# Kernel optimization log

Hardware: AMD Instinct MI355X
Metric: run time of the kernel (lower is better)

The kernel has to match this reference:

```python
import jax, jax.numpy as jnp
import numpy as np

D, L, C, CP, H, HD, QB, KB = 8, 2048, 128, 16, 4, 32, 32, 128
NQ = L // QB

def _ln(x, eps=1e-5):
    m = jnp.mean(x, axis=-1, keepdims=True)
    v = jnp.var(x, axis=-1, keepdims=True)
    return (x - m) * jax.lax.rsqrt(v + eps)

def _ada_ln(a, s, Wg, bg, Ws):
    # AF3 AdaLN: gated layernorm conditioned on s
    an = _ln(a); sn = _ln(s)
    return jax.nn.sigmoid(sn @ Wg + bg) * an + sn @ Ws

def setup_inputs() -> dict:
    key = jax.random.key(0)
    ks = jax.random.split(key, 32)
    p = lambda i, shape: jax.random.normal(ks[i], shape, dtype=jnp.float32) * 0.02
    inp = {}
    inp['A_I'] = jax.random.normal(ks[0], (D, L, C), dtype=jnp.float32)
    inp['S_I'] = jax.random.normal(ks[1], (D, L, C), dtype=jnp.float32)
    inp['Z_II'] = jax.random.normal(ks[2], (1, L, L, CP), dtype=jnp.float32)
    # static sliding-window indices: 128-key window centered on each 32-query block
    inp['indicesQ'] = jnp.arange(L, dtype=jnp.int64).reshape(NQ, QB)
    kraw = (jnp.arange(NQ) * QB - (KB - QB) // 2)[:, None] + jnp.arange(KB)[None, :]
    inp['indicesK'] = jnp.clip(kraw, 0, L - 1).astype(jnp.int64)
    inp['maskQ_float'] = jnp.zeros((NQ, QB), jnp.float32)
    inp['maskK_float'] = ((kraw < 0) | (kraw >= L)).astype(jnp.float32)
    # parameters
    inp['ada1_Wg'] = p(3, (C, C)); inp['ada1_bg'] = jnp.zeros((C,), jnp.float32); inp['ada1_Ws'] = p(4, (C, C))
    inp['Wq'] = p(5, (C, H * HD)); inp['bq'] = jnp.zeros((H * HD,), jnp.float32)
    inp['Wk'] = p(6, (C, H * HD)); inp['Wv'] = p(7, (C, H * HD))
    inp['ln0_g'] = jnp.ones((CP,), jnp.float32); inp['ln0_b'] = jnp.zeros((CP,), jnp.float32)
    inp['Wb'] = p(8, (CP, H))
    inp['Wg_attn'] = p(9, (C, H * HD))
    inp['Wa'] = p(10, (H * HD, C))
    inp['Wop'] = p(11, (C, C)); inp['bop'] = jnp.full((C,), -2.0, jnp.float32)
    inp['ada2_Wg'] = p(12, (C, C)); inp['ada2_bg'] = jnp.zeros((C,), jnp.float32); inp['ada2_Ws'] = p(13, (C, C))
    inp['W_sw'] = p(14, (C, 2 * C)); inp['W_lin'] = p(15, (C, 2 * C))
    inp['ct_Wg'] = p(16, (C, C)); inp['ct_bg'] = jnp.full((C,), -2.0, jnp.float32)
    inp['W_out2'] = p(17, (2 * C, C))
    return inp

def _forward(A_I, S_I, Z_II, indicesQ, indicesK, maskQ_float, maskK_float,
             ada1_Wg, ada1_bg, ada1_Ws, Wq, bq, Wk, Wv, ln0_g, ln0_b, Wb,
             Wg_attn, Wa, Wop, bop, ada2_Wg, ada2_bg, ada2_Ws, W_sw, W_lin,
             ct_Wg, ct_bg, W_out2):
    Dn, Lv = A_I.shape[0], A_I.shape[1]
    An = _ada_ln(A_I, S_I, ada1_Wg, ada1_bg, ada1_Ws)
    Q = (An @ Wq + bq).reshape(Dn, Lv, H, HD)
    K = (An @ Wk).reshape(Dn, Lv, H, HD)
    V = (An @ Wv).reshape(Dn, Lv, H, HD)
    B = ((_ln(Z_II) * ln0_g + ln0_b) @ Wb)[0]        # [L, L, H]
    G = jax.nn.sigmoid(An @ Wg_attn).reshape(Dn, Lv, H, HD)
    qs = Q[:, indicesQ]                              # [D, nq, qb, H, hd]
    ksub = K[:, indicesK]                            # [D, nq, kb, H, hd]
    vs = V[:, indicesK]
    attn = jnp.einsum('dnihc,dnjhc->dnijh', qs, ksub) / jnp.sqrt(jnp.float32(HD))
    bias = B[indicesQ[:, :, None], indicesK[:, None, :]]  # [nq, qb, kb, H]
    attn = attn + bias[None]
    mask = maskQ_float[None, :, :, None, None] + maskK_float[None, :, None, :, None]
    attn = attn - 1e9 * mask
    attn = jax.nn.softmax(attn, axis=-2)             # softmax over key window (j)
    af = jnp.einsum('dnijh,dnjhc->dnihc', attn, vs)
    af = af * (1.0 - maskQ_float)[None, :, :, None, None]
    af = af.reshape(Dn, -1, H, HD)[:, :Lv]
    af = (G * af).reshape(Dn, Lv, H * HD) @ Wa
    B_I = jax.nn.sigmoid(S_I @ Wop + bop) * af
    A = A_I + B_I
    an2 = _ada_ln(A, S_I, ada2_Wg, ada2_bg, ada2_Ws)
    b = jax.nn.silu(an2 @ W_sw) * (an2 @ W_lin)      # SwiGLU transition
    A = A + jax.nn.sigmoid(S_I @ ct_Wg + ct_bg) * (b @ W_out2)
    return A

def reference(A_I, S_I, Z_II, indicesQ, indicesK, maskQ_float, maskK_float,
              ada1_Wg, ada1_bg, ada1_Ws, Wq, bq, Wk, Wv, ln0_g, ln0_b, Wb,
              Wg_attn, Wa, Wop, bop, ada2_Wg, ada2_bg, ada2_Ws, W_sw, W_lin,
              ct_Wg, ct_bg, W_out2):
    return _forward(A_I, S_I, Z_II, indicesQ, indicesK, maskQ_float, maskK_float,
                    ada1_Wg, ada1_bg, ada1_Ws, Wq, bq, Wk, Wv, ln0_g, ln0_b, Wb,
                    Wg_attn, Wa, Wop, bop, ada2_Wg, ada2_bg, ada2_Ws, W_sw, W_lin,
                    ct_Wg, ct_bg, W_out2)
```

## Files before the change

### kernel.cpp

```cpp
#include <hip/hip_runtime.h>

#define DL 16384
#define LL 2048
#define NQB 64
#define QBS 32
#define KBS 128

typedef __attribute__((ext_vector_type(8))) short short8;
typedef __attribute__((ext_vector_type(4))) short short4v;
typedef __attribute__((ext_vector_type(4))) float f32x4;

__device__ __forceinline__ float sigmoidf_(float x) { return 1.f / (1.f + expf(-x)); }

__device__ __forceinline__ short f2bf(float f) {
    union { float f; unsigned u; } v; v.f = f;
    unsigned r = (v.u + 0x7FFFu + ((v.u >> 16) & 1u)) >> 16;
    return (short)r;
}
__device__ __forceinline__ float bf2f(short h) {
    union { unsigned u; float f; } v; v.u = ((unsigned)(unsigned short)h) << 16;
    return v.f;
}
__device__ __forceinline__ unsigned packbf16(short a, short b) {
    return ((unsigned)(unsigned short)a) | (((unsigned)(unsigned short)b) << 16);
}

#define AFRAG(buf, stride, r0, kk) (*(const short8*)&(buf)[(size_t)((r0) + cl) * (stride) + (kk) * 32 + kg * 8])
#define WFRAG(Wt, K, n0, kk) (*(const short8*)((Wt) + (size_t)((n0) + cl) * (K) + (kk) * 32 + kg * 8))
#define MFMA(acc, a, b) acc = __builtin_amdgcn_mfma_f32_16x16x32_bf16(a, b, acc, 0, 0, 0)

__global__ __launch_bounds__(256) void k_prep(
    const float* __restrict__ W0, const float* __restrict__ W1, const float* __restrict__ W2,
    const float* __restrict__ W3, const float* __restrict__ W4, const float* __restrict__ W5,
    const float* __restrict__ W6, const float* __restrict__ W7, const float* __restrict__ W8,
    const float* __restrict__ W9, const float* __restrict__ W10,
    const float* __restrict__ Wsw, const float* __restrict__ Wlin, const float* __restrict__ Wout2,
    const float* __restrict__ Z, const float* __restrict__ g16, const float* __restrict__ b16,
    const float* __restrict__ Wb,
    short* __restrict__ wout, short* __restrict__ BBt)
{
    __shared__ float sW[128 * 128];
    __shared__ float sWb[64], sg[16], sb[16];
    __shared__ short sT[4 * 4 * 128];
    const int b = blockIdx.x;
    const int tid = threadIdx.x;

    if (b < 17) {
        const float* srcs[14] = {W0,W1,W2,W3,W4,W5,W6,W7,W8,W9,W10,Wsw,Wlin,Wout2};
        const int sel[17]  = {0,1,2,3,4,5,6,7,8,9,10,11,11,12,12,13,13};
        const int soff[17] = {0,0,0,0,0,0,0,0,0,0,0, 0,128, 0,128, 0,16384};
        const int sN[17]   = {128,128,128,128,128,128,128,128,128,128,128, 256,256,256,256, 128,128};
        const int doff[17] = {0,16384,32768,49152,65536,81920,98304,114688,131072,147456,163840,
                              180224,196608, 212992,229376, 245760,245888};
        const int dK[17]   = {128,128,128,128,128,128,128,128,128,128,128, 128,128,128,128, 256,256};
        const float* src = srcs[sel[b]] + soff[b];
        const int srcN = sN[b];
        short* dst = wout + doff[b];
        const int dstK = dK[b];
        {
            const int r = tid >> 1, ch = (tid & 1) * 64;
            #pragma unroll
            for (int u = 0; u < 16; ++u) {
                float4 v = *(const float4*)(src + (size_t)r * srcN + ch + u * 4);
                *(float4*)&sW[r * 128 + ch + u * 4] = v;
            }
        }
        __syncthreads();
        {
            const int o = tid >> 1, kh = (tid & 1) * 64;
            #pragma unroll
            for (int u8 = 0; u8 < 8; ++u8) {
                short8 pk;
                #pragma unroll
                for (int e = 0; e < 8; ++e)
                    pk[e] = f2bf(sW[(kh + u8 * 8 + e) * 128 + o]);
                *(short8*)(dst + (size_t)o * dstK + kh + u8 * 8) = pk;
            }
        }
    } else {
        const int bb = b - 17;
        const int n = bb >> 3;
        const int io = (bb & 7) * 4;
        if (tid < 64) sWb[tid] = Wb[tid];
        if (tid < 16) { sg[tid] = g16[tid]; sb[tid] = b16[tid]; }
        __syncthreads();
        #pragma unroll
        for (int p = 0; p < 2; ++p) {
            int pair = tid + 256 * p;
            int il = pair >> 7, j = pair & 127;
            int i = io + il;
            int kr = n * 32 - 48 + j;
            int kc = min(max(kr, 0), LL - 1);
            const float4* z4 = (const float4*)(Z + ((long)(n * 32 + i) * LL + kc) * 16);
            float zv[16];
            #pragma unroll
            for (int w = 0; w < 4; ++w) {
                float4 v = z4[w];
                zv[w * 4 + 0] = v.x; zv[w * 4 + 1] = v.y; zv[w * 4 + 2] = v.z; zv[w * 4 + 3] = v.w;
            }
            float sm = 0.f, sq = 0.f;
            #pragma unroll
            for (int cp = 0; cp < 16; ++cp) { sm += zv[cp]; sq = fmaf(zv[cp], zv[cp], sq); }
            float m = sm * (1.f / 16.f);
            float rs = rsqrtf(sq * (1.f / 16.f) - m * m + 1e-5f);
            float b0 = 0.f, b1 = 0.f, b2 = 0.f, b3 = 0.f;
            #pragma unroll
            for (int cp = 0; cp < 16; ++cp) {
                float zn = (zv[cp] - m) * rs * sg[cp] + sb[cp];
                b0 = fmaf(zn, sWb[cp * 4 + 0], b0);
                b1 = fmaf(zn, sWb[cp * 4 + 1], b1);
                b2 = fmaf(zn, sWb[cp * 4 + 2], b2);
                b3 = fmaf(zn, sWb[cp * 4 + 3], b3);
            }
            sT[(0 * 4 + il) * 128 + j] = f2bf(b0);
            sT[(1 * 4 + il) * 128 + j] = f2bf(b1);
            sT[(2 * 4 + il) * 128 + j] = f2bf(b2);
            sT[(3 * 4 + il) * 128 + j] = f2bf(b3);
        }
        __syncthreads();
        #pragma unroll
        for (int rr = 0; rr < 2; ++rr) {
            int cid = tid + rr * 256;
            int hh = cid >> 7, rem = cid & 127;
            int il = rem >> 5, jb = (rem & 31) * 4;
            short4v pk = *(const short4v*)&sT[(hh * 4 + il) * 128 + jb];
            *(short4v*)(BBt + (((size_t)n * 4 + hh) * 32 + io + il) * 128 + jb) = pk;
        }
    }
}

__global__ __launch_bounds__(512) void k_adaln_qkvg(
    const float* __restrict__ A_I, const float* __restrict__ S_I,
    const short* __restrict__ Wg1t, const short* __restrict__ Ws1t,
    const short* __restrict__ Wqt, const short* __restrict__ Wkt,
    const short* __restrict__ Wvt, const short* __restrict__ Wgat,
    const float* __restrict__ bg1, const float* __restrict__ bq,
    short* __restrict__ Qo, short* __restrict__ Ko, short* __restrict__ Vo, short* __restrict__ Go)
{
    __shared__ short sAr[32 * 136];
    __shared__ short sSn[32 * 136];
    __shared__ short sAn[32 * 136];
    __shared__ float sMean[32], sRstd[32];
    const int tid = threadIdx.x;
    const int lane = tid & 63;
    const long t0 = (long)blockIdx.x * 32;

    {
        const int row = tid >> 4, seg = tid & 15;
        const float* ap = A_I + (t0 + row) * 128 + seg * 8;
        const float* sp = S_I + (t0 + row) * 128 + seg * 8;
        float av[8], sv[8];
        #pragma unroll
        for (int u = 0; u < 2; ++u) {
            float4 a4 = ((const float4*)ap)[u];
            float4 s4 = ((const float4*)sp)[u];
            av[4*u] = a4.x; av[4*u+1] = a4.y; av[4*u+2] = a4.z; av[4*u+3] = a4.w;
            sv[4*u] = s4.x; sv[4*u+1] = s4.y; sv[4*u+2] = s4.z; sv[4*u+3] = s4.w;
        }
        float am = 0.f, aq = 0.f, sm = 0.f, sq = 0.f;
        #pragma unroll
        for (int u = 0; u < 8; ++u) {
            am += av[u]; aq = fmaf(av[u], av[u], aq);
            sm += sv[u]; sq = fmaf(sv[u], sv[u], sq);
        }
        am += __shfl_xor(am, 1); am += __shfl_xor(am, 2); am += __shfl_xor(am, 4); am += __shfl_xor(am, 8);
        aq += __shfl_xor(aq, 1); aq += __shfl_xor(aq, 2); aq += __shfl_xor(aq, 4); aq += __shfl_xor(aq, 8);
        sm += __shfl_xor(sm, 1); sm += __shfl_xor(sm, 2); sm += __shfl_xor(sm, 4); sm += __shfl_xor(sm, 8);
        sq += __shfl_xor(sq, 1); sq += __shfl_xor(sq, 2); sq += __shfl_xor(sq, 4); sq += __shfl_xor(sq, 8);
        float amean = am * (1.f / 128.f);
        float arstd = rsqrtf(aq * (1.f / 128.f) - amean * amean + 1e-5f);
        float smean = sm * (1.f / 128.f);
        float srstd = rsqrtf(sq * (1.f / 128.f) - smean * smean + 1e-5f);
        if ((tid & 15) == 0) { sMean[row] = amean; sRstd[row] = arstd; }
        short8 pa, ps;
        #pragma unroll
        for (int e = 0; e < 8; ++e) {
            pa[e] = f2bf(av[e]);
            ps[e] = f2bf((sv[e] - smean) * srstd);
        }
        *(short8*)&sAr[row * 136 + seg * 8] = pa;
        *(short8*)&sSn[row * 136 + seg * 8] = ps;
    }
    __syncthreads();
    const int w = tid >> 6;
    const int n0 = w * 16;
    const int cl = lane & 15, kg = lane >> 4;
    {
        short8 wg[4], wsf[4];
        #pragma unroll
        for (int kk = 0; kk < 4; ++kk) {
            wg[kk]  = WFRAG(Wg1t, 128, n0, kk);
            wsf[kk] = WFRAG(Ws1t, 128, n0, kk);
        }
        #pragma unroll
        for (int mt = 0; mt < 2; ++mt) {
            f32x4 ag = {0.f, 0.f, 0.f, 0.f}, as = {0.f, 0.f, 0.f, 0.f};
            #pragma unroll
            for (int kk = 0; kk < 4; ++kk) {
                short8 a = AFRAG(sSn, 136, mt * 16, kk);
                MFMA(ag, wg[kk], a);
                MFMA(as, wsf[kk], a);
            }
            const int tok = mt * 16 + cl;
            const int c0 = n0 + kg * 4;
            float4 bg4 = *(const float4*)&bg1[c0];
            float mean = sMean[tok], rstd = sRstd[tok];
            short4v ar4 = *(const short4v*)&sAr[tok * 136 + c0];
            short4v o;
            #pragma unroll
            for (int i = 0; i < 4; ++i) {
                float an = (bf2f(ar4[i]) - mean) * rstd;
                float An = sigmoidf_(ag[i] + ((const float*)&bg4)[i]) * an + as[i];
                o[i] = f2bf(An);
            }
            *(short4v*)&sAn[tok * 136 + c0] = o;
        }
    }
    __syncthreads();
    {
        const float SCL = 0.17677669529663687f;
        short8 af[2][4];
        #pragma unroll
        for (int mt = 0; mt < 2; ++mt)
            #pragma unroll
            for (int kk = 0; kk < 4; ++kk)
                af[mt][kk] = AFRAG(sAn, 136, mt * 16, kk);
        const int c0 = n0 + kg * 4;
        float4 bq4 = *(const float4*)&bq[c0];
        #pragma unroll
        for (int m = 0; m < 4; ++m) {
            const short* Wt = (m == 0) ? Wqt : (m == 1) ? Wkt : (m == 2) ? Wvt : Wgat;
            short8 wf[4];
            #pragma unroll
            for (int kk = 0; kk < 4; ++kk) wf[kk] = WFRAG(Wt, 128, n0, kk);
            #pragma unroll
            for (int mt = 0; mt < 2; ++mt) {
                f32x4 acc = {0.f, 0.f, 0.f, 0.f};
                #pragma unroll
                for (int kk = 0; kk < 4; ++kk) MFMA(acc, wf[kk], af[mt][kk]);
                long t = t0 + mt * 16 + cl;
                short4v o;
                if (m == 0) {
                    #pragma unroll
                    for (int i = 0; i < 4; ++i) o[i] = f2bf((acc[i] + ((const float*)&bq4)[i]) * SCL);
                    *(short4v*)(Qo + t * 128 + c0) = o;
                } else if (m == 1) {
                    #pragma unroll
                    for (int i = 0; i < 4; ++i) o[i] = f2bf(acc[i]);
                    *(short4v*)(Ko + t * 128 + c0) = o;
                } else if (m == 2) {
                    #pragma unroll
                    for (int i = 0; i < 4; ++i) o[i] = f2bf(acc[i]);
                    *(short4v*)(Vo + t * 128 + c0) = o;
                } else {
                    #pragma unroll
                    for (int i = 0; i < 4; ++i) o[i] = f2bf(sigmoidf_(acc[i]));
                    *(short4v*)(Go + t * 128 + c0) = o;
                }
            }
        }
    }
}

__global__ __launch_bounds__(512) void k_attn_postf(
    const short* __restrict__ Qg, const short* __restrict__ Kg, const short* __restrict__ Vg,
    const short* __restrict__ Gg, const short* __restrict__ BBt, const float* __restrict__ maskK,
    const float* __restrict__ S_I, const float* __restrict__ A_I,
    const short* __restrict__ Wat, const short* __restrict__ Wopt, const short* __restrict__ ctWgt,
    const short* __restrict__ Wg2t, const short* __restrict__ Ws2t,
    const short* __restrict__ Wswt, const short* __restrict__ Wlint, const short* __restrict__ Wout2t,
    const float* __restrict__ bop, const float* __restrict__ ctbg, const float* __restrict__ bg2,
    float* __restrict__ Out)
{
    __shared__ __align__(16) char smem[78336];
    short* sAF  = (short*)smem;
    short* vts  = (short*)(smem + 8704);
    short* Pl   = (short*)(smem + 43520);
    short* sS   = (short*)(smem + 8704);
    short* sSn  = (short*)(smem + 17408);
    float* sA   = (float*)(smem + 26112);
    float* sMean = (float*)(smem + 43008);
    float* sRstd = (float*)(smem + 43136);
    short* sAn2 = sAF;
    short* sB   = (short*)(smem + 8704);

    const int n = blockIdx.x, d = blockIdx.y;
    const int tid = threadIdx.x;
    const int lane = tid & 63;
    const long tb = (long)d * LL;
    const long t0 = tb + n * 32;
    const int kbase = n * 32 - 48;
    const int cl = lane & 15, kg = lane >> 4;
    const int w = tid >> 6;
    const int h = w >> 1, amt = w & 1;

    {
        const int unit = tid >> 1, half = tid & 1;
        const int hh = unit >> 6, j0 = (unit & 63) * 2;
        int kc0 = min(max(kbase + j0, 0), LL - 1);
        int kc1 = min(max(kbase + j0 + 1, 0), LL - 1);
        const short8* p0 = (const short8*)(Vg + (tb + kc0) * 128 + hh * 32 + half * 16);
        const short8* p1 = (const short8*)(Vg + (tb + kc1) * 128 + hh * 32 + half * 16);
        short8 e0 = p0[0], e1 = p0[1];
        short8 o0 = p1[0], o1 = p1[1];
        short* vh = vts + hh * 4352;
        #pragma unroll
        for (int e = 0; e < 8; ++e)
            *(unsigned*)&vh[(half * 16 + e) * 136 + j0] = packbf16(e0[e], o0[e]);
        #pragma unroll
        for (int e = 0; e < 8; ++e)
            *(unsigned*)&vh[(half * 16 + 8 + e) * 136 + j0] = packbf16(e1[e], o1[e]);
    }

    float sc[8][4];
    {
        short8 qf = *(const short8*)(Qg + (t0 + amt * 16 + cl) * 128 + h * 32 + kg * 8);
        #pragma unroll
        for (int nt = 0; nt < 8; ++nt) {
            int kc = min(max(kbase + nt * 16 + cl, 0), LL - 1);
            short8 kf = *(const short8*)(Kg + (tb + kc) * 128 + h * 32 + kg * 8);
            f32x4 s = {0.f, 0.f, 0.f, 0.f};
            MFMA(s, kf, qf);
            float4 mk4 = *(const float4*)(maskK + n * 128 + nt * 16 + kg * 4);
            short4v bfr = *(const short4v*)(BBt + (((size_t)n * 4 + h) * 32 + amt * 16 + cl) * 128 + nt * 16 + kg * 4);
            #pragma unroll
            for (int i = 0; i < 4; ++i)
                sc[nt][i] = s[i] + bf2f(bfr[i]) - ((const float*)&mk4)[i] * 1e9f;
        }
    }
    {
        float mx = sc[0][0];
        #pragma unroll
        for (int nt = 0; nt < 8; ++nt)
            #pragma unroll
            for (int i = 0; i < 4; ++i) mx = fmaxf(mx, sc[nt][i]);
        mx = fmaxf(mx, __shfl_xor(mx, 16));
        mx = fmaxf(mx, __shfl_xor(mx, 32));
        float sm = 0.f;
        #pragma unroll
        for (int nt = 0; nt < 8; ++nt)
            #pragma unroll
            for (int i = 0; i < 4; ++i) {
                float p = __expf(sc[nt][i] - mx);
                sc[nt][i] = p; sm += p;
            }
        sm += __shfl_xor(sm, 16);
        sm += __shfl_xor(sm, 32);
        float inv = 1.f / sm;
        short* PH = Pl + h * 4352;
        const int tok = amt * 16 + cl;
        #pragma unroll
        for (int nt = 0; nt < 8; ++nt) {
            short4v p4;
            #pragma unroll
            for (int i = 0; i < 4; ++i) p4[i] = f2bf(sc[nt][i] * inv);
            *(short4v*)&PH[tok * 136 + nt * 16 + kg * 4] = p4;
        }
    }
    __syncthreads();
    {
        short* PH = Pl + h * 4352;
        short* vh = vts + h * 4352;
        const int tok = amt * 16 + cl;
        short8 pfr[4];
        #pragma unroll
        for (int kk = 0; kk < 4; ++kk)
            pfr[kk] = *(const short8*)&PH[tok * 136 + kk * 32 + kg * 8];
        #pragma unroll
        for (int ct = 0; ct < 2; ++ct) {
            f32x4 acc = {0.f, 0.f, 0.f, 0.f};
            #pragma unroll
            for (int kk = 0; kk < 4; ++kk) {
                short8 a = *(const short8*)&vh[(ct * 16 + cl) * 136 + kk * 32 + kg * 8];
                MFMA(acc, a, pfr[kk]);
            }
            const int c0 = h * 32 + ct * 16 + kg * 4;
            short4v g4 = *(const short4v*)(Gg + (t0 + tok) * 128 + c0);
            short4v o4;
            #pragma unroll
            for (int i = 0; i < 4; ++i) o4[i] = f2bf(bf2f(g4[i]) * acc[i]);
            *(short4v*)&sAF[tok * 136 + c0] = o4;
        }
    }
    __syncthreads();

    {
        const int row = tid >> 4, seg = tid & 15;
        const float* apI = A_I + (t0 + row) * 128 + seg * 8;
        #pragma unroll
        for (int u = 0; u < 2; ++u)
            *(float4*)&sA[row * 132 + seg * 8 + u * 4] = ((const float4*)apI)[u];
        const float* sp = S_I + (t0 + row) * 128 + seg * 8;
        float sv[8];
        #pragma unroll
        for (int u = 0; u < 2; ++u) {
            float4 s4 = ((const float4*)sp)[u];
            sv[4*u] = s4.x; sv[4*u+1] = s4.y; sv[4*u+2] = s4.z; sv[4*u+3] = s4.w;
        }
        float sm = 0.f, sq = 0.f;
        #pragma unroll
        for (int u = 0; u < 8; ++u) { sm += sv[u]; sq = fmaf(sv[u], sv[u], sq); }
        sm += __shfl_xor(sm, 1); sm += __shfl_xor(sm, 2); sm += __shfl_xor(sm, 4); sm += __shfl_xor(sm, 8);
        sq += __shfl_xor(sq, 1); sq += __shfl_xor(sq, 2); sq += __shfl_xor(sq, 4); sq += __shfl_xor(sq, 8);
        float smean = sm * (1.f / 128.f);
        float srstd = rsqrtf(sq * (1.f / 128.f) - smean * smean + 1e-5f);
        short8 pr, pn;
        #pragma unroll
        for (int e = 0; e < 8; ++e) {
            float s = sv[e];
            pr[e] = f2bf(s);
            pn[e] = f2bf((s - smean) * srstd);
        }
        *(short8*)&sS [row * 136 + seg * 8] = pr;
        *(short8*)&sSn[row * 136 + seg * 8] = pn;
    }
    __syncthreads();
    const int n0 = w * 16;
    const int c0 = n0 + kg * 4;
    float g2s[8];

    {
        short8 wA[4], wO[4], wG[4];
        #pragma unroll
        for (int kk = 0; kk < 4; ++kk) {
            wA[kk] = WFRAG(Wat, 128, n0, kk);
            wO[kk] = WFRAG(Wopt, 128, n0, kk);
            wG[kk] = WFRAG(ctWgt, 128, n0, kk);
        }
        float4 bop4 = *(const float4*)&bop[c0];
        float4 ct4  = *(const float4*)&ctbg[c0];
        #pragma unroll
        for (int rt = 0; rt < 2; ++rt) {
            f32x4 aA = {0.f,0.f,0.f,0.f}, aO = {0.f,0.f,0.f,0.f}, aG = {0.f,0.f,0.f,0.f};
            #pragma unroll
            for (int kk = 0; kk < 4; ++kk) {
                short8 af = AFRAG(sAF, 136, rt * 16, kk);
                short8 sf = AFRAG(sS, 136, rt * 16, kk);
                MFMA(aA, wA[kk], af);
                MFMA(aO, wO[kk], sf);
                MFMA(aG, wG[kk], sf);
            }
            const int tok = rt * 16 + cl;
            float4 Av = *(const float4*)&sA[tok * 132 + c0];
            float4 outv;
            #pragma unroll
            for (int i = 0; i < 4; ++i) {
                ((float*)&outv)[i] = ((const float*)&Av)[i]
                    + sigmoidf_(aO[i] + ((const float*)&bop4)[i]) * aA[i];
                g2s[rt * 4 + i] = sigmoidf_(aG[i] + ((const float*)&ct4)[i]);
            }
            *(float4*)&sA[tok * 132 + c0] = outv;
        }
    }
    __syncthreads();
    {
        const int row = tid >> 4, seg = tid & 15;
        float m = 0.f, q = 0.f;
        #pragma unroll
        for (int u = 0; u < 2; ++u) {
            float4 v = *(const float4*)&sA[row * 132 + seg * 8 + u * 4];
            m += v.x + v.y + v.z + v.w;
            q = fmaf(v.x, v.x, q); q = fmaf(v.y, v.y, q);
            q = fmaf(v.z, v.z, q); q = fmaf(v.w, v.w, q);
        }
        m += __shfl_xor(m, 1); m += __shfl_xor(m, 2); m += __shfl_xor(m, 4); m += __shfl_xor(m, 8);
        q += __shfl_xor(q, 1); q += __shfl_xor(q, 2); q += __shfl_xor(q, 4); q += __shfl_xor(q, 8);
        float mean = m * (1.f / 128.f);
        float rstd = rsqrtf(q * (1.f / 128.f) - mean * mean + 1e-5f);
        if ((tid & 15) == 0) { sMean[row] = mean; sRstd[row] = rstd; }
    }
    __syncthreads();
    {
        short8 wg2[4], ws2[4];
        #pragma unroll
        for (int kk = 0; kk < 4; ++kk) {
            wg2[kk] = WFRAG(Wg2t, 128, n0, kk);
            ws2[kk] = WFRAG(Ws2t, 128, n0, kk);
        }
        float4 bg24 = *(const float4*)&bg2[c0];
        #pragma unroll
        for (int rt = 0; rt < 2; ++rt) {
            f32x4 ag = {0.f,0.f,0.f,0.f}, as = {0.f,0.f,0.f,0.f};
            #pragma unroll
            for (int kk = 0; kk < 4; ++kk) {
                short8 a = AFRAG(sSn, 136, rt * 16, kk);
                MFMA(ag, wg2[kk], a);
                MFMA(as, ws2[kk], a);
            }
            const int tok = rt * 16 + cl;
            float mean = sMean[tok], rstd = sRstd[tok];
            float4 Av = *(const float4*)&sA[tok * 132 + c0];
            short4v o;
            #pragma unroll
            for (int i = 0; i < 4; ++i) {
                float lnA = (((const float*)&Av)[i] - mean) * rstd;
                o[i] = f2bf(sigmoidf_(ag[i] + ((const float*)&bg24)[i]) * lnA + as[i]);
            }
            *(short4v*)&sAn2[tok * 136 + c0] = o;
        }
    }
    __syncthreads();
    {
        short8 a2f[2][4];
        #pragma unroll
        for (int rt = 0; rt < 2; ++rt)
            #pragma unroll
            for (int kk = 0; kk < 4; ++kk)
                a2f[rt][kk] = AFRAG(sAn2, 136, rt * 16, kk);
        #pragma unroll
        for (int j = 0; j < 2; ++j) {
            const int n0b = w * 32 + j * 16;
            short8 ww[4], wl[4];
            #pragma unroll
            for (int kk = 0; kk < 4; ++kk) {
                ww[kk] = WFRAG(Wswt, 128, n0b, kk);
                wl[kk] = WFRAG(Wlint, 128, n0b, kk);
            }
            #pragma unroll
            for (int rt = 0; rt < 2; ++rt) {
                f32x4 aw = {0.f,0.f,0.f,0.f}, al = {0.f,0.f,0.f,0.f};
                #pragma unroll
                for (int kk = 0; kk < 4; ++kk) {
                    MFMA(aw, ww[kk], a2f[rt][kk]);
                    MFMA(al, wl[kk], a2f[rt][kk]);
                }
                const int tok = rt * 16 + cl;
                short4v o;
                #pragma unroll
                for (int i = 0; i < 4; ++i) {
                    float x = aw[i];
                    o[i] = f2bf((x / (1.f + expf(-x))) * al[i]);
                }
                *(short4v*)&sB[tok * 264 + n0b + kg * 4] = o;
            }
        }
    }
    __syncthreads();
    {
        short8 wo[8];
        #pragma unroll
        for (int kk = 0; kk < 8; ++kk) wo[kk] = WFRAG(Wout2t, 256, n0, kk);
        #pragma unroll
        for (int rt = 0; rt < 2; ++rt) {
            f32x4 acc = {0.f,0.f,0.f,0.f};
            #pragma unroll
            for (int kk = 0; kk < 8; ++kk) {
                short8 a = AFRAG(sB, 264, rt * 16, kk);
                MFMA(acc, wo[kk], a);
            }
            const int tok = rt * 16 + cl;
            float4 Av = *(const float4*)&sA[tok * 132 + c0];
            float4 outv;
            #pragma unroll
            for (int i = 0; i < 4; ++i)
                ((float*)&outv)[i] = ((const float*)&Av)[i] + g2s[rt * 4 + i] * acc[i];
            *(float4*)(Out + (t0 + tok) * 128 + c0) = outv;
        }
    }
}

extern "C" void kernel_launch(void* const* d_in, const int* in_sizes, int n_in,
                              void* d_out, int out_size, void* d_ws, size_t ws_size,
                              hipStream_t stream)
{
    const float* A_I  = (const float*)d_in[0];
    const float* S_I  = (const float*)d_in[1];
    const float* Z    = (const float*)d_in[2];
    const float* maskK = (const float*)d_in[6];
    const float* a1Wg = (const float*)d_in[7];
    const float* a1bg = (const float*)d_in[8];
    const float* a1Ws = (const float*)d_in[9];
    const float* Wq   = (const float*)d_in[10];
    const float* bq   = (const float*)d_in[11];
    const float* Wk   = (const float*)d_in[12];
    const float* Wv   = (const float*)d_in[13];
    const float* ln0g = (const float*)d_in[14];
    const float* ln0b = (const float*)d_in[15];
    const float* Wb   = (const float*)d_in[16];
    const float* Wga  = (const float*)d_in[17];
    const float* Wa   = (const float*)d_in[18];
    const float* Wop  = (const float*)d_in[19];
    const float* bop  = (const float*)d_in[20];
    const float* a2Wg = (const float*)d_in[21];
    const float* a2bg = (const float*)d_in[22];
    const float* a2Ws = (const float*)d_in[23];
    const float* Wsw  = (const float*)d_in[24];
    const float* Wlin = (const float*)d_in[25];
    const float* ctWg = (const float*)d_in[26];
    const float* ctbg = (const float*)d_in[27];
    const float* Wout2 = (const float*)d_in[28];
    float* out = (float*)d_out;

    const size_t NTC = (size_t)DL * 128;
    short* Qb = (short*)d_ws;
    short* Kb = Qb + NTC;
    short* Vb = Kb + NTC;
    short* Gb = Vb + NTC;
    short* BBt = Gb + NTC;
    short* wbt = BBt + (size_t)NQB * 4 * 32 * 128;

    short* Wg1t = wbt + 0 * 16384;
    short* Ws1t = wbt + 1 * 16384;
    short* Wqt  = wbt + 2 * 16384;
    short* Wkt  = wbt + 3 * 16384;
    short* Wvt  = wbt + 4 * 16384;
    short* Wgat = wbt + 5 * 16384;
    short* Wat  = wbt + 6 * 16384;
    short* Wopt = wbt + 7 * 16384;
    short* ctWgt = wbt + 8 * 16384;
    short* Wg2t = wbt + 9 * 16384;
    short* Ws2t = wbt + 10 * 16384;
    short* Wswt = wbt + 180224;
    short* Wlint = wbt + 212992;
    short* Wout2t = wbt + 245760;

    k_prep<<<529, 256, 0, stream>>>(a1Wg, a1Ws, Wq, Wk, Wv, Wga, Wa, Wop, ctWg,
                                    a2Wg, a2Ws, Wsw, Wlin, Wout2,
                                    Z, ln0g, ln0b, Wb, wbt, BBt);
    k_adaln_qkvg<<<DL / 32, 512, 0, stream>>>(A_I, S_I, Wg1t, Ws1t, Wqt, Wkt, Wvt, Wgat,
                                              a1bg, bq, Qb, Kb, Vb, Gb);
    k_attn_postf<<<dim3(NQB, 8), 512, 0, stream>>>(Qb, Kb, Vb, Gb, BBt, maskK,
                                                   S_I, A_I,
                                                   Wat, Wopt, ctWgt, Wg2t, Ws2t,
                                                   Wswt, Wlint, Wout2t,
                                                   bop, ctbg, a2bg, out);
}
```

Measured before the change: 71.22 us.

## Move pair-bias computation into the AdaLN/QKVG kernel and split off weight transpose

Splits the prep kernel in two. A small 17-block kernel now only transposes the weights. The Z pair-bias work (layernorm over 16 channels plus projection to 4 heads) moves into the AdaLN/QKV kernel as extra blocks 512..1023, using 512 threads per block with one pair per thread. The aim is to let the bias work overlap with the QKV projection and to shorten the serial prep kernel, though the extra blocks may compete for occupancy with the main work.

```diff
diff --git a/kernel.cpp b/kernel.cpp
--- a/kernel.cpp
+++ b/kernel.cpp
@@ -29,65 +29,80 @@
 #define WFRAG(Wt, K, n0, kk) (*(const short8*)((Wt) + (size_t)((n0) + cl) * (K) + (kk) * 32 + kg * 8))
 #define MFMA(acc, a, b) acc = __builtin_amdgcn_mfma_f32_16x16x32_bf16(a, b, acc, 0, 0, 0)
 
-__global__ __launch_bounds__(256) void k_prep(
+__global__ __launch_bounds__(256) void k_wtrans(
     const float* __restrict__ W0, const float* __restrict__ W1, const float* __restrict__ W2,
     const float* __restrict__ W3, const float* __restrict__ W4, const float* __restrict__ W5,
     const float* __restrict__ W6, const float* __restrict__ W7, const float* __restrict__ W8,
     const float* __restrict__ W9, const float* __restrict__ W10,
     const float* __restrict__ Wsw, const float* __restrict__ Wlin, const float* __restrict__ Wout2,
+    short* __restrict__ wout)
+{
+    __shared__ float sW[128 * 128];
+    const int b = blockIdx.x;
+    const int tid = threadIdx.x;
+    const float* srcs[14] = {W0,W1,W2,W3,W4,W5,W6,W7,W8,W9,W10,Wsw,Wlin,Wout2};
+    const int sel[17]  = {0,1,2,3,4,5,6,7,8,9,10,11,11,12,12,13,13};
+    const int soff[17] = {0,0,0,0,0,0,0,0,0,0,0, 0,128, 0,128, 0,16384};
+    const int sN[17]   = {128,128,128,128,128,128,128,128,128,128,128, 256,256,256,256, 128,128};
+    const int doff[17] = {0,16384,32768,49152,65536,81920,98304,114688,131072,147456,163840,
+                          180224,196608, 212992,229376, 245760,245888};
+    const int dK[17]   = {128,128,128,128,128,128,128,128,128,128,128, 128,128,128,128, 256,256};
+    const float* src = srcs[sel[b]] + soff[b];
+    const int srcN = sN[b];
+    short* dst = wout + doff[b];
+    const int dstK = dK[b];
+    {
+        const int r = tid >> 1, ch = (tid & 1) * 64;
+        #pragma unroll
+        for (int u = 0; u < 16; ++u) {
+            float4 v = *(const float4*)(src + (size_t)r * srcN + ch + u * 4);
+            *(float4*)&sW[r * 128 + ch + u * 4] = v;
+        }
+    }
+    __syncthreads();
+    {
+        const int o = tid >> 1, kh = (tid & 1) * 64;
+        #pragma unroll
+        for (int u8 = 0; u8 < 8; ++u8) {
+            short8 pk;
+            #pragma unroll
+            for (int e = 0; e < 8; ++e)
+                pk[e] = f2bf(sW[(kh + u8 * 8 + e) * 128 + o]);
+            *(short8*)(dst + (size_t)o * dstK + kh + u8 * 8) = pk;
+        }
+    }
+}
+
+__global__ __launch_bounds__(512) void k_main(
+    const float* __restrict__ A_I, const float* __restrict__ S_I,
+    const short* __restrict__ Wg1t, const short* __restrict__ Ws1t,
+    const short* __restrict__ Wqt, const short* __restrict__ Wkt,
+    const short* __restrict__ Wvt, const short* __restrict__ Wgat,
+    const float* __restrict__ bg1, const float* __restrict__ bq,
     const float* __restrict__ Z, const float* __restrict__ g16, const float* __restrict__ b16,
     const float* __restrict__ Wb,
-    short* __restrict__ wout, short* __restrict__ BBt)
+    short* __restrict__ Qo, short* __restrict__ Ko, short* __restrict__ Vo, short* __restrict__ Go,
+    short* __restrict__ BBt)
 {
-    __shared__ float sW[128 * 128];
+    __shared__ short sAr[32 * 136];
+    __shared__ short sSn[32 * 136];
+    __shared__ short sAn[32 * 136];
+    __shared__ float sMean[32], sRstd[32];
     __shared__ float sWb[64], sg[16], sb[16];
     __shared__ short sT[4 * 4 * 128];
-    const int b = blockIdx.x;
+    const int bid = blockIdx.x;
     const int tid = threadIdx.x;
-
-    if (b < 17) {
-        const float* srcs[14] = {W0,W1,W2,W3,W4,W5,W6,W7,W8,W9,W10,Wsw,Wlin,Wout2};
-        const int sel[17]  = {0,1,2,3,4,5,6,7,8,9,10,11,11,12,12,13,13};
-        const int soff[17] = {0,0,0,0,0,0,0,0,0,0,0, 0,128, 0,128, 0,16384};
-        const int sN[17]   = {128,128,128,128,128,128,128,128,128,128,128, 256,256,256,256, 128,128};
-        const int doff[17] = {0,16384,32768,49152,65536,81920,98304,114688,131072,147456,163840,
-                              180224,196608, 212992,229376, 245760,245888};
-        const int dK[17]   = {128,128,128,128,128,128,128,128,128,128,128, 128,128,128,128, 256,256};
-        const float* src = srcs[sel[b]] + soff[b];
-        const int srcN = sN[b];
-        short* dst = wout + doff[b];
-        const int dstK = dK[b];
-        {
-            const int r = tid >> 1, ch = (tid & 1) * 64;
-            #pragma unroll
-            for (int u = 0; u < 16; ++u) {
-                float4 v = *(const float4*)(src + (size_t)r * srcN + ch + u * 4);
-                *(float4*)&sW[r * 128 + ch + u * 4] = v;
-            }
-        }
-        __syncthreads();
-        {
-            const int o = tid >> 1, kh = (tid & 1) * 64;
-            #pragma unroll
-            for (int u8 = 0; u8 < 8; ++u8) {
-                short8 pk;
-                #pragma unroll
-                for (int e = 0; e < 8; ++e)
-                    pk[e] = f2bf(sW[(kh + u8 * 8 + e) * 128 + o]);
-                *(short8*)(dst + (size_t)o * dstK + kh + u8 * 8) = pk;
-            }
-        }
-    } else {
-        const int bb = b - 17;
+    const int lane = tid & 63;
+
+    if (bid >= 512) {
+        const int bb = bid - 512;
         const int n = bb >> 3;
         const int io = (bb & 7) * 4;
         if (tid < 64) sWb[tid] = Wb[tid];
         if (tid < 16) { sg[tid] = g16[tid]; sb[tid] = b16[tid]; }
         __syncthreads();
-        #pragma unroll
-        for (int p = 0; p < 2; ++p) {
-            int pair = tid + 256 * p;
-            int il = pair >> 7, j = pair & 127;
+        {
+            int il = tid >> 7, j = tid & 127;
             int i = io + il;
             int kr = n * 32 - 48 + j;
             int kc = min(max(kr, 0), LL - 1);
@@ -118,33 +133,16 @@
             sT[(3 * 4 + il) * 128 + j] = f2bf(b3);
         }
         __syncthreads();
-        #pragma unroll
-        for (int rr = 0; rr < 2; ++rr) {
-            int cid = tid + rr * 256;
-            int hh = cid >> 7, rem = cid & 127;
+        {
+            int hh = tid >> 7, rem = tid & 127;
             int il = rem >> 5, jb = (rem & 31) * 4;
             short4v pk = *(const short4v*)&sT[(hh * 4 + il) * 128 + jb];
             *(short4v*)(BBt + (((size_t)n * 4 + hh) * 32 + io + il) * 128 + jb) = pk;
         }
-    }
-}
-
-__global__ __launch_bounds__(512) void k_adaln_qkvg(
-    const float* __restrict__ A_I, const float* __restrict__ S_I,
-    const short* __restrict__ Wg1t, const short* __restrict__ Ws1t,
-    const short* __restrict__ Wqt, const short* __restrict__ Wkt,
-    const short* __restrict__ Wvt, const short* __restrict__ Wgat,
-    const float* __restrict__ bg1, const float* __restrict__ bq,
-    short* __restrict__ Qo, short* __restrict__ Ko, short* __restrict__ Vo, short* __restrict__ Go)
-{
-    __shared__ short sAr[32 * 136];
-    __shared__ short sSn[32 * 136];
-    __shared__ short sAn[32 * 136];
-    __shared__ float sMean[32], sRstd[32];
-    const int tid = threadIdx.x;
-    const int lane = tid & 63;
-    const long t0 = (long)blockIdx.x * 32;
-
+        return;
+    }
+
+    const long t0 = (long)bid * 32;
     {
         const int row = tid >> 4, seg = tid & 15;
         const float* ap = A_I + (t0 + row) * 128 + seg * 8;
@@ -614,11 +612,11 @@
     short* Wlint = wbt + 212992;
     short* Wout2t = wbt + 245760;
 
-    k_prep<<<529, 256, 0, stream>>>(a1Wg, a1Ws, Wq, Wk, Wv, Wga, Wa, Wop, ctWg,
-                                    a2Wg, a2Ws, Wsw, Wlin, Wout2,
-                                    Z, ln0g, ln0b, Wb, wbt, BBt);
-    k_adaln_qkvg<<<DL / 32, 512, 0, stream>>>(A_I, S_I, Wg1t, Ws1t, Wqt, Wkt, Wvt, Wgat,
-                                              a1bg, bq, Qb, Kb, Vb, Gb);
+    k_wtrans<<<17, 256, 0, stream>>>(a1Wg, a1Ws, Wq, Wk, Wv, Wga, Wa, Wop, ctWg,
+                                     a2Wg, a2Ws, Wsw, Wlin, Wout2, wbt);
+    k_main<<<1024, 512, 0, stream>>>(A_I, S_I, Wg1t, Ws1t, Wqt, Wkt, Wvt, Wgat,
+                                     a1bg, bq, Z, ln0g, ln0b, Wb,
+                                     Qb, Kb, Vb, Gb, BBt);
     k_attn_postf<<<dim3(NQB, 8), 512, 0, stream>>>(Qb, Kb, Vb, Gb, BBt, maskK,
                                                    S_I, A_I,
                                                    Wat, Wopt, ctWgt, Wg2t, Ws2t,
```

Measured after the change: 69.36 us. 2.6% less time.
